# Kernel optimization log

Hardware: AMD Instinct MI355X
Metric: run time of the kernel (lower is better)

The kernel has to match this reference:

```python
import jax, jax.numpy as jnp
import numpy as np


def setup_inputs() -> dict:
    key = jax.random.key(0)
    x = jax.random.uniform(key, (16, 3, 224, 224), dtype=jnp.float32)
    return {"x": x, "timesteps": 32, "burst_length": 3, "interburst_interval": 5}


def reference(x, timesteps, burst_length, interburst_interval):
    period = burst_length + interburst_interval  # 8
    max_bursts = timesteps // period             # 4
    x_norm = jnp.clip(x, 0.0, 1.0)
    # floor(x * max_bursts) == torch .long() cast for non-negative values
    n_bursts = jnp.floor(x_norm * max_bursts)    # [B, *input_shape], float

    t = jnp.arange(timesteps)                    # [T]
    burst_idx = (t // period).astype(x.dtype)    # which burst each timestep belongs to
    within_burst = (t % period) < burst_length   # [T] bool

    # reshape time axis to broadcast at position 1: [1, T, 1, ..., 1]
    tshape = (1, timesteps) + (1,) * (x.ndim - 1)
    burst_idx = burst_idx.reshape(tshape)
    within_burst = within_burst.reshape(tshape)

    nb = jnp.expand_dims(n_bursts, 1)            # [B, 1, *input_shape]
    spikes = (within_burst & (burst_idx < nb)).astype(jnp.float32)
    return spikes  # [B, T, *input_shape]
```

## Files before the change

kernel.cpp:

```cpp
#include <hip/hip_runtime.h>


__global__ __launch_bounds__(256) void burst_coding_kernel(
    const float* __restrict__ x, float* __restrict__ out,
    const int* __restrict__ p_bl, const int* __restrict__ p_ibi,
    int T, int S4, long total4)
{
    const int bl     = *p_bl;
    const int period = bl + *p_ibi;
    const int maxb   = T / period;
    const float mbf  = (float)maxb;

    for (long i = blockIdx.x * (long)blockDim.x + threadIdx.x; i < total4;
         i += (long)gridDim.x * blockDim.x) {
        const long b  = i / S4;
        const int  s4 = (int)(i - b * S4);

        const float4 xv = reinterpret_cast<const float4*>(x)[i];

        const int n0 = (int)(fminf(fmaxf(xv.x, 0.f), 1.f) * mbf);
        const int n1 = (int)(fminf(fmaxf(xv.y, 0.f), 1.f) * mbf);
        const int n2 = (int)(fminf(fmaxf(xv.z, 0.f), 1.f) * mbf);
        const int n3 = (int)(fminf(fmaxf(xv.w, 0.f), 1.f) * mbf);

        float4* outp = reinterpret_cast<float4*>(out) + b * (long)T * S4 + s4;

        int tmod = 0, bidx = 0;
        for (int t = 0; t < T; ++t) {
            const bool w = (tmod < bl);
            float4 v;
            v.x = (w && (bidx < n0)) ? 1.f : 0.f;
            v.y = (w && (bidx < n1)) ? 1.f : 0.f;
            v.z = (w && (bidx < n2)) ? 1.f : 0.f;
            v.w = (w && (bidx < n3)) ? 1.f : 0.f;
            outp[(long)t * S4] = v;
            if (++tmod == period) { tmod = 0; ++bidx; }
        }
    }
}

extern "C" void kernel_launch(void* const* d_in, const int* in_sizes, int n_in,
                              void* d_out, int out_size, void* d_ws, size_t ws_size,
                              hipStream_t stream) {
    const float* x   = (const float*)d_in[0];
    const int* p_bl  = (const int*)d_in[2];
    const int* p_ibi = (const int*)d_in[3];
    float* out = (float*)d_out;

    const long N  = (long)in_sizes[0];
    const int  T  = (int)((long)out_size / N);
    const int  S  = 3 * 224 * 224;
    const int  S4 = S / 4;
    const long total4 = N / 4;

    const int threads = 256;
    const long blocks = (total4 + threads - 1) / threads;

    burst_coding_kernel<<<dim3((unsigned)blocks), dim3(threads), 0, stream>>>(
        x, out, p_bl, p_ibi, T, S4, total4);
}
```

Baseline: 53.84 us.

## Parallelize over timesteps with 2D grid and skip input loads for silent steps

The grid changes from one thread per input float4 looping over all timesteps to a 2D grid where each thread writes a single output float4 for one (batch, timestep) pair. Timesteps outside a burst window, or past the maximum burst count, write zeros without reading the input. Active steps compare the clipped, scaled input against a float threshold instead of an integer burst count. This adds parallelism and makes each store one contiguous wave-wide write, at the cost of re-reading the input for every active timestep (mostly cache hits).

Measured after the change: 53.83 us. Within noise of the previous version (-0.0%).

```diff
diff --git a/kernel.cpp b/kernel.cpp
--- a/kernel.cpp
+++ b/kernel.cpp
@@ -4,39 +4,38 @@
 __global__ __launch_bounds__(256) void burst_coding_kernel(
     const float* __restrict__ x, float* __restrict__ out,
     const int* __restrict__ p_bl, const int* __restrict__ p_ibi,
-    int T, int S4, long total4)
+    int T, int S4)
 {
     const int bl     = *p_bl;
     const int period = bl + *p_ibi;
     const int maxb   = T / period;
+
+    const int bt   = blockIdx.y;
+    const int t    = bt % T;
+    const int b    = bt / T;
+    const int tm   = t % period;
+    const int bidx = t / period;
+
+    const int s4 = blockIdx.x * blockDim.x + threadIdx.x;
+    if (s4 >= S4) return;
+
+    float4* op = reinterpret_cast<float4*>(out) + (long)bt * S4 + s4;
+
+    if (tm >= bl || bidx >= maxb) {
+        *op = make_float4(0.f, 0.f, 0.f, 0.f);
+        return;
+    }
+
     const float mbf  = (float)maxb;
+    const float bthr = (float)(bidx + 1);
+    const float4 xv  = reinterpret_cast<const float4*>(x)[(long)b * S4 + s4];
 
-    for (long i = blockIdx.x * (long)blockDim.x + threadIdx.x; i < total4;
-         i += (long)gridDim.x * blockDim.x) {
-        const long b  = i / S4;
-        const int  s4 = (int)(i - b * S4);
-
-        const float4 xv = reinterpret_cast<const float4*>(x)[i];
-
-        const int n0 = (int)(fminf(fmaxf(xv.x, 0.f), 1.f) * mbf);
-        const int n1 = (int)(fminf(fmaxf(xv.y, 0.f), 1.f) * mbf);
-        const int n2 = (int)(fminf(fmaxf(xv.z, 0.f), 1.f) * mbf);
-        const int n3 = (int)(fminf(fmaxf(xv.w, 0.f), 1.f) * mbf);
-
-        float4* outp = reinterpret_cast<float4*>(out) + b * (long)T * S4 + s4;
-
-        int tmod = 0, bidx = 0;
-        for (int t = 0; t < T; ++t) {
-            const bool w = (tmod < bl);
-            float4 v;
-            v.x = (w && (bidx < n0)) ? 1.f : 0.f;
-            v.y = (w && (bidx < n1)) ? 1.f : 0.f;
-            v.z = (w && (bidx < n2)) ? 1.f : 0.f;
-            v.w = (w && (bidx < n3)) ? 1.f : 0.f;
-            outp[(long)t * S4] = v;
-            if (++tmod == period) { tmod = 0; ++bidx; }
-        }
-    }
+    float4 v;
+    v.x = (fminf(fmaxf(xv.x, 0.f), 1.f) * mbf >= bthr) ? 1.f : 0.f;
+    v.y = (fminf(fmaxf(xv.y, 0.f), 1.f) * mbf >= bthr) ? 1.f : 0.f;
+    v.z = (fminf(fmaxf(xv.z, 0.f), 1.f) * mbf >= bthr) ? 1.f : 0.f;
+    v.w = (fminf(fmaxf(xv.w, 0.f), 1.f) * mbf >= bthr) ? 1.f : 0.f;
+    *op = v;
 }
 
 extern "C" void kernel_launch(void* const* d_in, const int* in_sizes, int n_in,
@@ -51,11 +50,12 @@
     const int  T  = (int)((long)out_size / N);
     const int  S  = 3 * 224 * 224;
     const int  S4 = S / 4;
-    const long total4 = N / 4;
+    const int  B  = (int)(N / S);
 
     const int threads = 256;
-    const long blocks = (total4 + threads - 1) / threads;
+    dim3 grid((S4 + threads - 1) / threads,
+              (unsigned)(B * T));
 
-    burst_coding_kernel<<<dim3((unsigned)blocks), dim3(threads), 0, stream>>>(
-        x, out, p_bl, p_ibi, T, S4, total4);
+    burst_coding_kernel<<<grid, dim3(threads), 0, stream>>>(
+        x, out, p_bl, p_ibi, T, S4);
 }
```
